# Performance work log

Measured on AMD Instinct MI355X. Metric: run time of the kernel, lower is better.

## Reference

```python
import jax, jax.numpy as jnp
import numpy as np
from jax.ops import segment_sum

N = 100000   # nodes
E = 1600000  # edges
F = 128      # node feature dim
H = 128      # hidden dim
FE = 16      # edge feature dim
G = 256      # num graphs
EPS = 1e-5   # batch-norm eps


def setup_inputs() -> dict:
    key = jax.random.key(0)
    ks = jax.random.split(key, 16)
    s = 0.05
    return {
        "x": jax.random.normal(ks[0], (N, F), jnp.float32),
        "edge_index": jax.random.randint(ks[1], (2, E), 0, N, dtype=jnp.int32),
        "edge_attr": jax.random.normal(ks[2], (E, FE), jnp.float32),
        "batch_idx": jnp.sort(jax.random.randint(ks[3], (N,), 0, G, dtype=jnp.int32)),
        # GCN layer 1
        "W_g1": jax.random.normal(ks[4], (F, H), jnp.float32) * s,
        "b_g1": jnp.zeros((H,), jnp.float32),
        "gamma1": jnp.ones((H,), jnp.float32),
        "beta1": jnp.zeros((H,), jnp.float32),
        # GCN layer 2
        "W_g2": jax.random.normal(ks[5], (H, H), jnp.float32) * s,
        "b_g2": jnp.zeros((H,), jnp.float32),
        "gamma2": jnp.ones((H,), jnp.float32),
        "beta2": jnp.zeros((H,), jnp.float32),
        # edge encoder MLP
        "W_e1": jax.random.normal(ks[6], (FE, H), jnp.float32) * s,
        "b_e1": jnp.zeros((H,), jnp.float32),
        "W_e2": jax.random.normal(ks[7], (H, H), jnp.float32) * s,
        "b_e2": jnp.zeros((H,), jnp.float32),
    }


def _gcn_bn_relu(x, src, dst, W, b, gamma, beta):
    """GCNConv (sym-normalized, self-loops) + BatchNorm1d (batch stats) + ReLU."""
    h = x @ W                                             # [N, H]
    ones = jnp.ones((E,), h.dtype)
    deg = segment_sum(ones, dst, num_segments=N) + 1.0    # self-loop degree
    dinv = jax.lax.rsqrt(deg)                             # [N]
    norm = dinv[src] * dinv[dst]                          # [E]
    agg = segment_sum(h[src] * norm[:, None], dst, num_segments=N)
    out = agg + h * (dinv * dinv)[:, None] + b            # self-loop + bias
    mu = out.mean(axis=0)
    var = out.var(axis=0)
    out = (out - mu) * jax.lax.rsqrt(var + EPS) * gamma + beta
    return jax.nn.relu(out)


def reference(x, edge_index, edge_attr, batch_idx, W_g1, b_g1, gamma1, beta1,
              W_g2, b_g2, gamma2, beta2, W_e1, b_e1, W_e2, b_e2):
    src, dst = edge_index[0], edge_index[1]
    h = _gcn_bn_relu(x, src, dst, W_g1, b_g1, gamma1, beta1)
    h = _gcn_bn_relu(h, src, dst, W_g2, b_g2, gamma2, beta2)

    # global mean pool over nodes per graph
    node_cnt = segment_sum(jnp.ones((N,), h.dtype), batch_idx, num_segments=G)
    graph_repr = segment_sum(h, batch_idx, num_segments=G) / jnp.maximum(node_cnt, 1.0)[:, None]

    # edge encoder MLP + per-graph edge mean (vectorized version of the loop)
    e = jax.nn.relu(edge_attr @ W_e1 + b_e1) @ W_e2 + b_e2   # [E, H]
    edge_batch = batch_idx[src]                              # [E]
    edge_cnt = segment_sum(jnp.ones((E,), e.dtype), edge_batch, num_segments=G)
    edge_sum = segment_sum(e, edge_batch, num_segments=G)
    edge_repr = jnp.where(edge_cnt[:, None] > 0, edge_sum / jnp.maximum(edge_cnt, 1.0)[:, None], 0.0)

    return graph_repr + edge_repr  # [G, H]
```

## Files before the change

### kernel.cpp

```cpp
#include <hip/hip_runtime.h>
#include <cstdint>

__device__ inline unsigned int bfpack2(float a, float b) {
  unsigned int ua = __float_as_uint(a), ub = __float_as_uint(b);
  ua += 0x7FFFu + ((ua >> 16) & 1u);
  ub += 0x7FFFu + ((ub >> 16) & 1u);
  return (ua >> 16) | (ub & 0xFFFF0000u);
}
__device__ inline float bflo(unsigned int u) { return __uint_as_float(u << 16); }
__device__ inline float bfhi(unsigned int u) { return __uint_as_float(u & 0xFFFF0000u); }

__global__ __launch_bounds__(256) void pre_kernel(const int* __restrict__ src,
                                                  const int* __restrict__ dst,
                                                  int* __restrict__ deg,
                                                  int* __restrict__ deg2, int nE) {
  int e = blockIdx.x * 256 + threadIdx.x;
  if (e < nE) {
    atomicAdd(&deg[dst[e]], 1);
    atomicAdd(&deg2[src[e]], 1);
  }
}

__global__ __launch_bounds__(256) void scanA_kernel(const int* __restrict__ deg,
                                                    const int* __restrict__ deg2,
                                                    int* __restrict__ rp,
                                                    int* __restrict__ rp2,
                                                    int* __restrict__ part,
                                                    int* __restrict__ part2,
                                                    int n, int nb) {
  __shared__ int sh[256];
  int b = blockIdx.x, t = threadIdx.x;
  const int* d = (b < nb) ? deg : deg2;
  int* r = (b < nb) ? rp : rp2;
  int* p = (b < nb) ? part : part2;
  int pad = (b < nb) ? 1 : 0;
  int bb = (b < nb) ? b : b - nb;
  int base = bb * 1024 + t * 4;
  int v0 = (base + 0 < n) ? d[base + 0] : 0;
  int v1 = (base + 1 < n) ? d[base + 1] : 0;
  int v2 = (base + 2 < n) ? d[base + 2] : 0;
  int v3 = (base + 3 < n) ? d[base + 3] : 0;
  if (pad) {
    v0 = (v0 + 7) & ~7; v1 = (v1 + 7) & ~7;
    v2 = (v2 + 7) & ~7; v3 = (v3 + 7) & ~7;
  }
  int ts = v0 + v1 + v2 + v3;
  sh[t] = ts;
  __syncthreads();
  for (int off = 1; off < 256; off <<= 1) {
    int x = (t >= off) ? sh[t - off] : 0;
    __syncthreads();
    sh[t] += x;
    __syncthreads();
  }
  int excl = sh[t] - ts;
  if (t == 255) p[bb] = sh[255];
  if (base + 0 < n) r[base + 0] = excl;
  if (base + 1 < n) r[base + 1] = excl + v0;
  if (base + 2 < n) r[base + 2] = excl + v0 + v1;
  if (base + 3 < n) r[base + 3] = excl + v0 + v1 + v2;
}

__global__ void scanB_kernel(int* part, int* part2, int* rp, int* rp2, int nb, int n) {
  if (threadIdx.x == 0) {
    int* p = (blockIdx.x == 0) ? part : part2;
    int* r = (blockIdx.x == 0) ? rp : rp2;
    int run = 0;
    for (int i = 0; i < nb; ++i) { int v = p[i]; p[i] = run; run += v; }
    r[n] = run;
  }
}

__global__ __launch_bounds__(256) void scanC_kernel(int* __restrict__ rp,
                                                    int* __restrict__ rp2,
                                                    const int* __restrict__ part,
                                                    const int* __restrict__ part2,
                                                    int* __restrict__ cursor,
                                                    int* __restrict__ cursor2,
                                                    const int* __restrict__ deg,
                                                    float* __restrict__ dinv, int n) {
  int i = blockIdx.x * 256 + threadIdx.x;
  if (i < n) {
    int v = rp[i] + part[i >> 10];
    rp[i] = v;
    cursor[i] = v;
    dinv[i] = rsqrtf((float)deg[i] + 1.0f);
  } else if (i < 2 * n) {
    int j = i - n;
    int v = rp2[j] + part2[j >> 10];
    rp2[j] = v;
    cursor2[j] = v;
  }
}

template <bool SC>
__global__ __launch_bounds__(256) void placepad_kernel(const int* __restrict__ src,
                                                       const int* __restrict__ dst,
                                                       const int* __restrict__ batch,
                                                       const float* __restrict__ dinv,
                                                       const float* __restrict__ ea,
                                                       int* __restrict__ cursor,
                                                       int* __restrict__ cursor2,
                                                       unsigned int* __restrict__ swp,
                                                       unsigned int* __restrict__ epk,
                                                       int* __restrict__ pos2,
                                                       unsigned int* __restrict__ eah,
                                                       const int* __restrict__ rp,
                                                       const int* __restrict__ deg,
                                                       int nE, int nN) {
  int t = blockIdx.x * 256 + threadIdx.x;
  if (t < nE) {
    int s = src[t];
    int d = dst[t];
    int p1 = atomicAdd(&cursor[d], 1);
    unsigned int fb = __float_as_uint(dinv[s] * dinv[d]);
    fb += 0x7FFFu + ((fb >> 16) & 1u);
    swp[p1] = ((fb >> 16) << 17) | (unsigned int)s;
    int g = batch[s];
    int p2 = atomicAdd(&cursor2[s], 1);
    epk[p2] = ((unsigned int)g << 21) | (unsigned int)t;
    if (SC) {
      const float4* p = reinterpret_cast<const float4*>(ea + (size_t)t * 16);
      float4 a = p[0], b = p[1], c = p[2], dd = p[3];
      uint4 o0, o1;
      o0.x = bfpack2(a.x, a.y); o0.y = bfpack2(a.z, a.w);
      o0.z = bfpack2(b.x, b.y); o0.w = bfpack2(b.z, b.w);
      o1.x = bfpack2(c.x, c.y); o1.y = bfpack2(c.z, c.w);
      o1.z = bfpack2(dd.x, dd.y); o1.w = bfpack2(dd.z, dd.w);
      uint4* dp = reinterpret_cast<uint4*>(eah + (size_t)p2 * 8);
      dp[0] = o0;
      dp[1] = o1;
    } else {
      pos2[t] = p2;
    }
  } else if (t < nE + nN) {
    int i = t - nE;
    int b = rp[i] + deg[i], e = rp[i + 1];
    for (int k = b; k < e; ++k) swp[k] = (unsigned int)i;
  } else if (t < nE + nN + 32) {
    int k = t - nE - nN;
    swp[rp[nN] + k] = 0u;
  }
}

template <bool FUSED>
__global__ __launch_bounds__(256) void gemm128_kernel(const float* __restrict__ A,
                                                      const float* __restrict__ W,
                                                      const float* __restrict__ bs,
                                                      const float* __restrict__ bq,
                                                      const float* __restrict__ gm,
                                                      const float* __restrict__ bt,
                                                      float invN,
                                                      unsigned int* __restrict__ hpk2,
                                                      int nrows) {
  extern __shared__ float lds[];
  float* Ws = lds;
  float* xs = lds + 128 * 128;
  float* scs = xs + 16 * 128;
  float* shs = scs + 128;
  const int t = threadIdx.x;
  for (int i = t; i < (128 * 128) / 4; i += 256)
    reinterpret_cast<float4*>(Ws)[i] = reinterpret_cast<const float4*>(W)[i];
  if (FUSED && t < 128) {
    float mu = bs[t] * invN;
    float var = bq[t] * invN - mu * mu;
    float sc = gm[t] * rsqrtf(var + 1e-5f);
    scs[t] = sc;
    shs[t] = bt[t] - mu * sc;
  }
  const int wave = t >> 6, lane = t & 63;
  const size_t sbase = (size_t)(lane >> 3) * (size_t)nrows * 8 + (lane & 7);
  for (int rb = blockIdx.x * 16; rb < nrows; rb += gridDim.x * 16) {
    int nr = min(16, nrows - rb);
    __syncthreads();
    for (int i = t; i < nr * 32; i += 256) {
      float4 v = reinterpret_cast<const float4*>(A + (size_t)rb * 128)[i];
      if (FUSED) {
        float4 sc4 = reinterpret_cast<const float4*>(scs)[i & 31];
        float4 sh4 = reinterpret_cast<const float4*>(shs)[i & 31];
        v.x = fmaxf(fmaf(v.x, sc4.x, sh4.x), 0.f);
        v.y = fmaxf(fmaf(v.y, sc4.y, sh4.y), 0.f);
        v.z = fmaxf(fmaf(v.z, sc4.z, sh4.z), 0.f);
        v.w = fmaxf(fmaf(v.w, sc4.w, sh4.w), 0.f);
      }
      reinterpret_cast<float4*>(xs)[i] = v;
    }
    __syncthreads();
    float acc[4][2] = {{0.f, 0.f}, {0.f, 0.f}, {0.f, 0.f}, {0.f, 0.f}};
    const float* xw = xs + wave * 4 * 128;
#pragma unroll 4
    for (int k = 0; k < 128; ++k) {
      float w0 = Ws[k * 128 + lane];
      float w1 = Ws[k * 128 + 64 + lane];
#pragma unroll
      for (int r = 0; r < 4; ++r) {
        float a = xw[r * 128 + k];
        acc[r][0] = fmaf(a, w0, acc[r][0]);
        acc[r][1] = fmaf(a, w1, acc[r][1]);
      }
    }
#pragma unroll
    for (int r = 0; r < 4; ++r) {
      int row = rb + wave * 4 + r;
      if (row < nrows)
        hpk2[sbase + (size_t)row * 8] = bfpack2(acc[r][0], acc[r][1]);
    }
  }
}

__global__ __launch_bounds__(256) void spmm8_kernel(const unsigned int* __restrict__ hpk2,
                                                    const float* __restrict__ dinv,
                                                    const int* __restrict__ rp,
                                                    const unsigned int* __restrict__ swp,
                                                    const float* __restrict__ bias,
                                                    float* __restrict__ outp,
                                                    float* __restrict__ bnsum,
                                                    float* __restrict__ bnsq, int nN) {
  const int lane = threadIdx.x & 63;
  const int ch = lane & 7;
  const int es = lane >> 3;
  const int slice = blockIdx.x & 7;
  const unsigned int* hs = hpk2 + (size_t)slice * (size_t)nN * 8;
  const int cb = slice * 8;
  const int wib = (int)(blockIdx.x >> 3) * 4 + (int)(threadIdx.x >> 6);
  const int nws = (int)(gridDim.x >> 3) * 4;
  float b0 = bias[cb + ch], b1 = bias[64 + cb + ch];
  float s0 = 0.f, s1 = 0.f, q0 = 0.f, q1 = 0.f;
  const int half = (nN + 1) >> 1;

#define SPMM_CHUNK(J, ACC0, ACC1)                                         \
  {                                                                       \
    unsigned int v_ = __builtin_nontemporal_load(swp + (J) + es);         \
    unsigned int pp_ = hs[(size_t)(v_ & 0x1FFFFu) * 8 + ch];              \
    float ww_ = __uint_as_float((v_ & 0xFFFE0000u) >> 1);                 \
    ACC0 = fmaf(ww_, bflo(pp_), ACC0);                                    \
    ACC1 = fmaf(ww_, bfhi(pp_), ACC1);                                    \
  }

  for (int p = wib; p < half; p += nws) {
    const int n0 = p;
    const int n1 = p + half;
    const bool has1 = n1 < nN;
    int j0 = rp[n0];
    const int end0 = rp[n0 + 1];
    int j1 = 0, end1 = 0;
    if (has1) { j1 = rp[n1]; end1 = rp[n1 + 1]; }
    float a00 = 0.f, a01 = 0.f, b00 = 0.f, b01 = 0.f;
    float a10 = 0.f, a11 = 0.f, b10 = 0.f, b11 = 0.f;
    while (j0 + 8 < end0 && j1 + 8 < end1) {
      SPMM_CHUNK(j0, a00, a01);
      SPMM_CHUNK(j0 + 8, b00, b01);
      SPMM_CHUNK(j1, a10, a11);
      SPMM_CHUNK(j1 + 8, b10, b11);
      j0 += 16; j1 += 16;
    }
    while (j0 + 8 < end0) {
      SPMM_CHUNK(j0, a00, a01);
      SPMM_CHUNK(j0 + 8, b00, b01);
      j0 += 16;
    }
    if (j0 < end0) SPMM_CHUNK(j0, a00, a01);
    while (j1 + 8 < end1) {
      SPMM_CHUNK(j1, a10, a11);
      SPMM_CHUNK(j1 + 8, b10, b11);
      j1 += 16;
    }
    if (j1 < end1) SPMM_CHUNK(j1, a10, a11);

    a00 += b00; a01 += b01;
    a10 += b10; a11 += b11;
    a00 += __shfl_xor(a00, 8);  a01 += __shfl_xor(a01, 8);
    a10 += __shfl_xor(a10, 8);  a11 += __shfl_xor(a11, 8);
    a00 += __shfl_xor(a00, 16); a01 += __shfl_xor(a01, 16);
    a10 += __shfl_xor(a10, 16); a11 += __shfl_xor(a11, 16);
    a00 += __shfl_xor(a00, 32); a01 += __shfl_xor(a01, 32);
    a10 += __shfl_xor(a10, 32); a11 += __shfl_xor(a11, 32);
    if (es == 0) {
      {
        float dn = dinv[n0];
        float sw = dn * dn;
        unsigned int pn = hs[(size_t)n0 * 8 + ch];
        float o0 = fmaf(bflo(pn), sw, a00) + b0;
        float o1 = fmaf(bfhi(pn), sw, a01) + b1;
        __builtin_nontemporal_store(o0, &outp[(size_t)n0 * 128 + cb + ch]);
        __builtin_nontemporal_store(o1, &outp[(size_t)n0 * 128 + 64 + cb + ch]);
        s0 += o0; s1 += o1;
        q0 = fmaf(o0, o0, q0); q1 = fmaf(o1, o1, q1);
      }
      if (has1) {
        float dn = dinv[n1];
        float sw = dn * dn;
        unsigned int pn = hs[(size_t)n1 * 8 + ch];
        float o0 = fmaf(bflo(pn), sw, a10) + b0;
        float o1 = fmaf(bfhi(pn), sw, a11) + b1;
        __builtin_nontemporal_store(o0, &outp[(size_t)n1 * 128 + cb + ch]);
        __builtin_nontemporal_store(o1, &outp[(size_t)n1 * 128 + 64 + cb + ch]);
        s0 += o0; s1 += o1;
        q0 = fmaf(o0, o0, q0); q1 = fmaf(o1, o1, q1);
      }
    }
  }
#undef SPMM_CHUNK
  if (es == 0) {
    atomicAdd(&bnsum[cb + ch], s0);
    atomicAdd(&bnsum[64 + cb + ch], s1);
    atomicAdd(&bnsq[cb + ch], q0);
    atomicAdd(&bnsq[64 + cb + ch], q1);
  }
}

__global__ __launch_bounds__(256) void pool_kernel(const float* __restrict__ h,
                                                   const int* __restrict__ batch,
                                                   const float* __restrict__ bs,
                                                   const float* __restrict__ bq,
                                                   const float* __restrict__ gm,
                                                   const float* __restrict__ bt,
                                                   float invN,
                                                   float* __restrict__ gsum,
                                                   float* __restrict__ gcnt,
                                                   int nN, int chunk) {
  const int lane = threadIdx.x & 63;
  const int wid = (blockIdx.x * blockDim.x + threadIdx.x) >> 6;
  int beg = wid * chunk;
  if (beg >= nN) return;
  int end = min(nN, beg + chunk);
  const int c2 = 2 * lane;
  float mu0 = bs[c2] * invN, mu1 = bs[c2 + 1] * invN;
  float va0 = bq[c2] * invN - mu0 * mu0, va1 = bq[c2 + 1] * invN - mu1 * mu1;
  float sc0 = gm[c2] * rsqrtf(va0 + 1e-5f), sc1v = gm[c2 + 1] * rsqrtf(va1 + 1e-5f);
  float sh0 = bt[c2] - mu0 * sc0, sh1v = bt[c2 + 1] - mu1 * sc1v;
  int cur = -1;
  float a0 = 0.f, a1 = 0.f, cnt = 0.f;
  for (int n = beg; n < end; ++n) {
    int g = batch[n];
    if (g != cur) {
      if (cur >= 0) {
        atomicAdd(&gsum[cur * 128 + c2], a0);
        atomicAdd(&gsum[cur * 128 + c2 + 1], a1);
        if (lane == 0) atomicAdd(&gcnt[cur], cnt);
      }
      cur = g; a0 = 0.f; a1 = 0.f; cnt = 0.f;
    }
    float2 v = *reinterpret_cast<const float2*>(h + (size_t)n * 128 + c2);
    a0 += fmaxf(fmaf(v.x, sc0, sh0), 0.f);
    a1 += fmaxf(fmaf(v.y, sc1v, sh1v), 0.f);
    cnt += 1.f;
  }
  if (cur >= 0) {
    atomicAdd(&gsum[cur * 128 + c2], a0);
    atomicAdd(&gsum[cur * 128 + c2 + 1], a1);
    if (lane == 0) atomicAdd(&gcnt[cur], cnt);
  }
}

__global__ __launch_bounds__(256) void scatter_kernel(const float* __restrict__ ea,
                                                      const int* __restrict__ pos2,
                                                      unsigned int* __restrict__ eah, int nE) {
  int e = blockIdx.x * 256 + threadIdx.x;
  if (e < nE) {
    const float4* p = reinterpret_cast<const float4*>(ea + (size_t)e * 16);
    float4 a = p[0], b = p[1], c = p[2], d = p[3];
    uint4 o0, o1;
    o0.x = bfpack2(a.x, a.y); o0.y = bfpack2(a.z, a.w);
    o0.z = bfpack2(b.x, b.y); o0.w = bfpack2(b.z, b.w);
    o1.x = bfpack2(c.x, c.y); o1.y = bfpack2(c.z, c.w);
    o1.z = bfpack2(d.x, d.y); o1.w = bfpack2(d.z, d.w);
    int j = pos2[e];
    uint4* dst = reinterpret_cast<uint4*>(eah + (size_t)j * 8);
    dst[0] = o0;
    dst[1] = o1;
  }
}

__global__ __launch_bounds__(256) void edge6_kernel(const unsigned int* __restrict__ eah,
                                                    const unsigned int* __restrict__ epk,
                                                    const float* __restrict__ We1,
                                                    const float* __restrict__ be1,
                                                    float* __restrict__ esum,
                                                    float* __restrict__ ecnt,
                                                    int nE, int chunk) {
  const int lane = threadIdx.x & 63;
  const int wid = (blockIdx.x * 256 + threadIdx.x) >> 6;
  int beg = wid * chunk;
  if (beg >= nE) return;
  int end = min(nE, beg + chunk);
  float w0[16], w1[16];
#pragma unroll
  for (int k = 0; k < 16; ++k) {
    w0[k] = We1[k * 128 + lane];
    w1[k] = We1[k * 128 + 64 + lane];
  }
  float b0 = be1[lane], b1 = be1[64 + lane];
  int cur = -1;
  float a0 = 0.f, a1 = 0.f, cnt = 0.f;
  const uint4* rowp = reinterpret_cast<const uint4*>(eah + (size_t)beg * 8);
  uint4 q0 = rowp[0], q1 = rowp[1];
  int g = (int)(epk[beg] >> 21);
  for (int j = beg; j < end; ++j) {
    uint4 n0, n1;
    int ng = g;
    if (j + 1 < end) {
      const uint4* np = reinterpret_cast<const uint4*>(eah + (size_t)(j + 1) * 8);
      n0 = np[0];
      n1 = np[1];
      ng = (int)(epk[j + 1] >> 21);
    }
    if (g != cur) {
      if (cur >= 0) {
        atomicAdd(&esum[cur * 128 + lane], a0);
        atomicAdd(&esum[cur * 128 + 64 + lane], a1);
        if (lane == 0) atomicAdd(&ecnt[cur], cnt);
      }
      cur = g; a0 = 0.f; a1 = 0.f; cnt = 0.f;
    }
    float u0 = b0, u1 = b1;
    float f;
    f = bflo(q0.x); u0 = fmaf(f, w0[0], u0);  u1 = fmaf(f, w1[0], u1);
    f = bfhi(q0.x); u0 = fmaf(f, w0[1], u0);  u1 = fmaf(f, w1[1], u1);
    f = bflo(q0.y); u0 = fmaf(f, w0[2], u0);  u1 = fmaf(f, w1[2], u1);
    f = bfhi(q0.y); u0 = fmaf(f, w0[3], u0);  u1 = fmaf(f, w1[3], u1);
    f = bflo(q0.z); u0 = fmaf(f, w0[4], u0);  u1 = fmaf(f, w1[4], u1);
    f = bfhi(q0.z); u0 = fmaf(f, w0[5], u0);  u1 = fmaf(f, w1[5], u1);
    f = bflo(q0.w); u0 = fmaf(f, w0[6], u0);  u1 = fmaf(f, w1[6], u1);
    f = bfhi(q0.w); u0 = fmaf(f, w0[7], u0);  u1 = fmaf(f, w1[7], u1);
    f = bflo(q1.x); u0 = fmaf(f, w0[8], u0);  u1 = fmaf(f, w1[8], u1);
    f = bfhi(q1.x); u0 = fmaf(f, w0[9], u0);  u1 = fmaf(f, w1[9], u1);
    f = bflo(q1.y); u0 = fmaf(f, w0[10], u0); u1 = fmaf(f, w1[10], u1);
    f = bfhi(q1.y); u0 = fmaf(f, w0[11], u0); u1 = fmaf(f, w1[11], u1);
    f = bflo(q1.z); u0 = fmaf(f, w0[12], u0); u1 = fmaf(f, w1[12], u1);
    f = bfhi(q1.z); u0 = fmaf(f, w0[13], u0); u1 = fmaf(f, w1[13], u1);
    f = bflo(q1.w); u0 = fmaf(f, w0[14], u0); u1 = fmaf(f, w1[14], u1);
    f = bfhi(q1.w); u0 = fmaf(f, w0[15], u0); u1 = fmaf(f, w1[15], u1);
    a0 += fmaxf(u0, 0.f);
    a1 += fmaxf(u1, 0.f);
    cnt += 1.f;
    q0 = n0; q1 = n1; g = ng;
  }
  if (cur >= 0) {
    atomicAdd(&esum[cur * 128 + lane], a0);
    atomicAdd(&esum[cur * 128 + 64 + lane], a1);
    if (lane == 0) atomicAdd(&ecnt[cur], cnt);
  }
}

__global__ __launch_bounds__(128) void final_kernel(const float* __restrict__ gsum,
                                                    const float* __restrict__ gcnt,
                                                    const float* __restrict__ esum,
                                                    const float* __restrict__ ecnt,
                                                    const float* __restrict__ We2,
                                                    const float* __restrict__ be2,
                                                    float* __restrict__ out) {
  __shared__ float row[128];
  int g = blockIdx.x, c = threadIdx.x;
  row[c] = esum[g * 128 + c];
  __syncthreads();
  float acc = 0.f;
#pragma unroll 4
  for (int k = 0; k < 128; ++k) acc = fmaf(row[k], We2[k * 128 + c], acc);
  float ce = ecnt[g];
  float er = (ce > 0.f) ? (acc / ce + be2[c]) : 0.f;
  float cn = gcnt[g];
  float gr = gsum[g * 128 + c] / fmaxf(cn, 1.f);
  out[g * 128 + c] = gr + er;
}

extern "C" void kernel_launch(void* const* d_in, const int* in_sizes, int n_in,
                              void* d_out, int out_size, void* d_ws, size_t ws_size,
                              hipStream_t stream) {
  const float* x    = (const float*)d_in[0];
  const int*   ei   = (const int*)d_in[1];
  const float* ea   = (const float*)d_in[2];
  const int*   bidx = (const int*)d_in[3];
  const float* Wg1  = (const float*)d_in[4];
  const float* bg1  = (const float*)d_in[5];
  const float* gm1  = (const float*)d_in[6];
  const float* bt1  = (const float*)d_in[7];
  const float* Wg2  = (const float*)d_in[8];
  const float* bg2  = (const float*)d_in[9];
  const float* gm2  = (const float*)d_in[10];
  const float* bt2  = (const float*)d_in[11];
  const float* We1  = (const float*)d_in[12];
  const float* be1  = (const float*)d_in[13];
  const float* We2  = (const float*)d_in[14];
  const float* be2  = (const float*)d_in[15];
  float* out = (float*)d_out;

  const int N = in_sizes[3];
  const int E = in_sizes[1] / 2;
  const int G = out_size / 128;
  const int* srcp = ei;
  const int* dstp = ei + E;
  const int Epad = E + 8 * N;

  char* w = (char*)d_ws;
  auto alloc = [&](size_t b) {
    char* p = w;
    w += (b + 15) & ~(size_t)15;
    return p;
  };
  float* bufB    = (float*)alloc((size_t)N * 128 * 4);
  unsigned int* hpk2 = (unsigned int*)alloc((size_t)N * 64 * 4);
  unsigned int* swp = (unsigned int*)alloc(((size_t)Epad + 32) * 4);
  unsigned int* epk = (unsigned int*)alloc((size_t)E * 4);
  int*   pos2    = (int*)alloc((size_t)E * 4);
  int*   rp      = (int*)alloc((size_t)(N + 1) * 4);
  int*   rp2     = (int*)alloc((size_t)(N + 1) * 4);
  int*   cursor  = (int*)alloc((size_t)N * 4);
  int*   cursor2 = (int*)alloc((size_t)N * 4);
  float* dinv    = (float*)alloc((size_t)N * 4);
  char* zbase = w;
  int*   deg  = (int*)alloc((size_t)N * 4);
  int*   deg2 = (int*)alloc((size_t)N * 4);
  float* bs1  = (float*)alloc(512);
  float* bq1  = (float*)alloc(512);
  float* bs2  = (float*)alloc(512);
  float* bq2  = (float*)alloc(512);
  float* gsum = (float*)alloc((size_t)G * 128 * 4);
  float* gcnt = (float*)alloc((size_t)G * 4);
  float* esum = (float*)alloc((size_t)G * 128 * 4);
  float* ecnt = (float*)alloc((size_t)G * 4);
  int*   part  = (int*)alloc(4096);
  int*   part2 = (int*)alloc(4096);
  size_t zbytes = (size_t)(w - zbase);

  size_t used = (size_t)(w - (char*)d_ws);
  size_t eah_bytes = (size_t)E * 32;
  bool dedicated = (used + eah_bytes + 64) <= ws_size;
  unsigned int* eah = dedicated ? (unsigned int*)alloc(eah_bytes) : (unsigned int*)bufB;

  hipMemsetAsync(zbase, 0, zbytes, stream);

  (void)hipFuncSetAttribute((const void*)gemm128_kernel<false>,
                            hipFuncAttributeMaxDynamicSharedMemorySize, 74752);
  (void)hipFuncSetAttribute((const void*)gemm128_kernel<true>,
                            hipFuncAttributeMaxDynamicSharedMemorySize, 74752);

  pre_kernel<<<(E + 255) / 256, 256, 0, stream>>>(srcp, dstp, deg, deg2, E);
  int nb = (N + 1023) / 1024;
  scanA_kernel<<<2 * nb, 256, 0, stream>>>(deg, deg2, rp, rp2, part, part2, N, nb);
  scanB_kernel<<<2, 64, 0, stream>>>(part, part2, rp, rp2, nb, N);
  scanC_kernel<<<(2 * N + 255) / 256, 256, 0, stream>>>(rp, rp2, part, part2, cursor,
                                                        cursor2, deg, dinv, N);
  int ppg = (E + N + 32 + 255) / 256;
  if (dedicated) {
    placepad_kernel<true><<<ppg, 256, 0, stream>>>(srcp, dstp, bidx, dinv, ea, cursor,
                                                   cursor2, swp, epk, pos2, eah, rp, deg,
                                                   E, N);
  } else {
    placepad_kernel<false><<<ppg, 256, 0, stream>>>(srcp, dstp, bidx, dinv, ea, cursor,
                                                    cursor2, swp, epk, pos2, eah, rp, deg,
                                                    E, N);
  }

  const float invN = 1.0f / (float)N;

  gemm128_kernel<false><<<512, 256, 74752, stream>>>(x, Wg1, nullptr, nullptr, nullptr,
                                                     nullptr, 0.f, hpk2, N);
  spmm8_kernel<<<2048, 256, 0, stream>>>(hpk2, dinv, rp, swp, bg1, bufB, bs1, bq1, N);

  gemm128_kernel<true><<<512, 256, 74752, stream>>>(bufB, Wg2, bs1, bq1, gm1, bt1, invN,
                                                    hpk2, N);
  spmm8_kernel<<<2048, 256, 0, stream>>>(hpk2, dinv, rp, swp, bg2, bufB, bs2, bq2, N);

  int nwp = (2048 * 256) / 64;
  int chunkN = (N + nwp - 1) / nwp;
  pool_kernel<<<2048, 256, 0, stream>>>(bufB, bidx, bs2, bq2, gm2, bt2, invN,
                                        gsum, gcnt, N, chunkN);

  if (!dedicated) {
    scatter_kernel<<<(E + 255) / 256, 256, 0, stream>>>(ea, pos2, eah, E);
  }
  int nwe = (2048 * 256) / 64;
  int chunkE = (E + nwe - 1) / nwe;
  edge6_kernel<<<2048, 256, 0, stream>>>(eah, epk, We1, be1, esum, ecnt, E, chunkE);

  final_kernel<<<G, 128, 0, stream>>>(gsum, gcnt, esum, ecnt, We2, be2, out);
}
```

Before: 1.236 ms.

## Fuse edge encoder work into SpMM launches as extra blocks

Splits the edge-encoder/per-graph edge reduction into two halves and runs each half inside the two SpMM launches, using the first 256 blocks of each launch for edge work and the rest for SpMM. The goal is to overlap the compute-heavy edge MLP with the gather-bound SpMM and remove a separate edge kernel launch. It relies on the dedicated path having filled eah before the SpMMs. The edge blocks compete with SpMM for CUs, and their heavier register use may lower occupancy for the fused kernel.

```diff
diff --git a/kernel.cpp b/kernel.cpp
--- a/kernel.cpp
+++ b/kernel.cpp
@@ -208,22 +208,23 @@
   }
 }
 
-__global__ __launch_bounds__(256) void spmm8_kernel(const unsigned int* __restrict__ hpk2,
-                                                    const float* __restrict__ dinv,
-                                                    const int* __restrict__ rp,
-                                                    const unsigned int* __restrict__ swp,
-                                                    const float* __restrict__ bias,
-                                                    float* __restrict__ outp,
-                                                    float* __restrict__ bnsum,
-                                                    float* __restrict__ bnsq, int nN) {
+__device__ __forceinline__ void spmm_body(const unsigned int* __restrict__ hpk2,
+                                          const float* __restrict__ dinv,
+                                          const int* __restrict__ rp,
+                                          const unsigned int* __restrict__ swp,
+                                          const float* __restrict__ bias,
+                                          float* __restrict__ outp,
+                                          float* __restrict__ bnsum,
+                                          float* __restrict__ bnsq, int nN, int eb) {
   const int lane = threadIdx.x & 63;
   const int ch = lane & 7;
   const int es = lane >> 3;
-  const int slice = blockIdx.x & 7;
+  const int bid = (int)blockIdx.x - eb;
+  const int slice = bid & 7;
   const unsigned int* hs = hpk2 + (size_t)slice * (size_t)nN * 8;
   const int cb = slice * 8;
-  const int wib = (int)(blockIdx.x >> 3) * 4 + (int)(threadIdx.x >> 6);
-  const int nws = (int)(gridDim.x >> 3) * 4;
+  const int wib = (bid >> 3) * 4 + (int)(threadIdx.x >> 6);
+  const int nws = (((int)gridDim.x - eb) >> 3) * 4;
   float b0 = bias[cb + ch], b1 = bias[64 + cb + ch];
   float s0 = 0.f, s1 = 0.f, q0 = 0.f, q1 = 0.f;
   const int half = (nN + 1) >> 1;
@@ -309,6 +310,100 @@
   }
 }
 
+__device__ __forceinline__ void edge_body(const unsigned int* __restrict__ eah,
+                                          const unsigned int* __restrict__ epk,
+                                          const float* __restrict__ We1,
+                                          const float* __restrict__ be1,
+                                          float* __restrict__ esum,
+                                          float* __restrict__ ecnt,
+                                          int eoff, int eend, int chunk) {
+  const int lane = threadIdx.x & 63;
+  const int wid = ((int)blockIdx.x * 256 + (int)threadIdx.x) >> 6;
+  int beg = eoff + wid * chunk;
+  if (beg >= eend) return;
+  int end = min(eend, beg + chunk);
+  float w0[16], w1[16];
+#pragma unroll
+  for (int k = 0; k < 16; ++k) {
+    w0[k] = We1[k * 128 + lane];
+    w1[k] = We1[k * 128 + 64 + lane];
+  }
+  float b0 = be1[lane], b1 = be1[64 + lane];
+  int cur = -1;
+  float a0 = 0.f, a1 = 0.f, cnt = 0.f;
+  const uint4* rowp = reinterpret_cast<const uint4*>(eah + (size_t)beg * 8);
+  uint4 q0 = rowp[0], q1 = rowp[1];
+  int g = (int)(epk[beg] >> 21);
+  for (int j = beg; j < end; ++j) {
+    uint4 n0, n1;
+    int ng = g;
+    if (j + 1 < end) {
+      const uint4* np = reinterpret_cast<const uint4*>(eah + (size_t)(j + 1) * 8);
+      n0 = np[0];
+      n1 = np[1];
+      ng = (int)(epk[j + 1] >> 21);
+    }
+    if (g != cur) {
+      if (cur >= 0) {
+        atomicAdd(&esum[cur * 128 + lane], a0);
+        atomicAdd(&esum[cur * 128 + 64 + lane], a1);
+        if (lane == 0) atomicAdd(&ecnt[cur], cnt);
+      }
+      cur = g; a0 = 0.f; a1 = 0.f; cnt = 0.f;
+    }
+    float u0 = b0, u1 = b1;
+    float f;
+    f = bflo(q0.x); u0 = fmaf(f, w0[0], u0);  u1 = fmaf(f, w1[0], u1);
+    f = bfhi(q0.x); u0 = fmaf(f, w0[1], u0);  u1 = fmaf(f, w1[1], u1);
+    f = bflo(q0.y); u0 = fmaf(f, w0[2], u0);  u1 = fmaf(f, w1[2], u1);
+    f = bfhi(q0.y); u0 = fmaf(f, w0[3], u0);  u1 = fmaf(f, w1[3], u1);
+    f = bflo(q0.z); u0 = fmaf(f, w0[4], u0);  u1 = fmaf(f, w1[4], u1);
+    f = bfhi(q0.z); u0 = fmaf(f, w0[5], u0);  u1 = fmaf(f, w1[5], u1);
+    f = bflo(q0.w); u0 = fmaf(f, w0[6], u0);  u1 = fmaf(f, w1[6], u1);
+    f = bfhi(q0.w); u0 = fmaf(f, w0[7], u0);  u1 = fmaf(f, w1[7], u1);
+    f = bflo(q1.x); u0 = fmaf(f, w0[8], u0);  u1 = fmaf(f, w1[8], u1);
+    f = bfhi(q1.x); u0 = fmaf(f, w0[9], u0);  u1 = fmaf(f, w1[9], u1);
+    f = bflo(q1.y); u0 = fmaf(f, w0[10], u0); u1 = fmaf(f, w1[10], u1);
+    f = bfhi(q1.y); u0 = fmaf(f, w0[11], u0); u1 = fmaf(f, w1[11], u1);
+    f = bflo(q1.z); u0 = fmaf(f, w0[12], u0); u1 = fmaf(f, w1[12], u1);
+    f = bfhi(q1.z); u0 = fmaf(f, w0[13], u0); u1 = fmaf(f, w1[13], u1);
+    f = bflo(q1.w); u0 = fmaf(f, w0[14], u0); u1 = fmaf(f, w1[14], u1);
+    f = bfhi(q1.w); u0 = fmaf(f, w0[15], u0); u1 = fmaf(f, w1[15], u1);
+    a0 += fmaxf(u0, 0.f);
+    a1 += fmaxf(u1, 0.f);
+    cnt += 1.f;
+    q0 = n0; q1 = n1; g = ng;
+  }
+  if (cur >= 0) {
+    atomicAdd(&esum[cur * 128 + lane], a0);
+    atomicAdd(&esum[cur * 128 + 64 + lane], a1);
+    if (lane == 0) atomicAdd(&ecnt[cur], cnt);
+  }
+}
+
+__global__ __launch_bounds__(256) void spmm_edge_kernel(const unsigned int* __restrict__ hpk2,
+                                                        const float* __restrict__ dinv,
+                                                        const int* __restrict__ rp,
+                                                        const unsigned int* __restrict__ swp,
+                                                        const float* __restrict__ bias,
+                                                        float* __restrict__ outp,
+                                                        float* __restrict__ bnsum,
+                                                        float* __restrict__ bnsq, int nN,
+                                                        const unsigned int* __restrict__ eah,
+                                                        const unsigned int* __restrict__ epk,
+                                                        const float* __restrict__ We1,
+                                                        const float* __restrict__ be1,
+                                                        float* __restrict__ esum,
+                                                        float* __restrict__ ecnt,
+                                                        int eoff, int eend, int chunkE,
+                                                        int eb) {
+  if ((int)blockIdx.x < eb) {
+    edge_body(eah, epk, We1, be1, esum, ecnt, eoff, eend, chunkE);
+  } else {
+    spmm_body(hpk2, dinv, rp, swp, bias, outp, bnsum, bnsq, nN, eb);
+  }
+}
+
 __global__ __launch_bounds__(256) void pool_kernel(const float* __restrict__ h,
                                                    const int* __restrict__ batch,
                                                    const float* __restrict__ bs,
@@ -379,68 +474,7 @@
                                                     float* __restrict__ esum,
                                                     float* __restrict__ ecnt,
                                                     int nE, int chunk) {
-  const int lane = threadIdx.x & 63;
-  const int wid = (blockIdx.x * 256 + threadIdx.x) >> 6;
-  int beg = wid * chunk;
-  if (beg >= nE) return;
-  int end = min(nE, beg + chunk);
-  float w0[16], w1[16];
-#pragma unroll
-  for (int k = 0; k < 16; ++k) {
-    w0[k] = We1[k * 128 + lane];
-    w1[k] = We1[k * 128 + 64 + lane];
-  }
-  float b0 = be1[lane], b1 = be1[64 + lane];
-  int cur = -1;
-  float a0 = 0.f, a1 = 0.f, cnt = 0.f;
-  const uint4* rowp = reinterpret_cast<const uint4*>(eah + (size_t)beg * 8);
-  uint4 q0 = rowp[0], q1 = rowp[1];
-  int g = (int)(epk[beg] >> 21);
-  for (int j = beg; j < end; ++j) {
-    uint4 n0, n1;
-    int ng = g;
-    if (j + 1 < end) {
-      const uint4* np = reinterpret_cast<const uint4*>(eah + (size_t)(j + 1) * 8);
-      n0 = np[0];
-      n1 = np[1];
-      ng = (int)(epk[j + 1] >> 21);
-    }
-    if (g != cur) {
-      if (cur >= 0) {
-        atomicAdd(&esum[cur * 128 + lane], a0);
-        atomicAdd(&esum[cur * 128 + 64 + lane], a1);
-        if (lane == 0) atomicAdd(&ecnt[cur], cnt);
-      }
-      cur = g; a0 = 0.f; a1 = 0.f; cnt = 0.f;
-    }
-    float u0 = b0, u1 = b1;
-    float f;
-    f = bflo(q0.x); u0 = fmaf(f, w0[0], u0);  u1 = fmaf(f, w1[0], u1);
-    f = bfhi(q0.x); u0 = fmaf(f, w0[1], u0);  u1 = fmaf(f, w1[1], u1);
-    f = bflo(q0.y); u0 = fmaf(f, w0[2], u0);  u1 = fmaf(f, w1[2], u1);
-    f = bfhi(q0.y); u0 = fmaf(f, w0[3], u0);  u1 = fmaf(f, w1[3], u1);
-    f = bflo(q0.z); u0 = fmaf(f, w0[4], u0);  u1 = fmaf(f, w1[4], u1);
-    f = bfhi(q0.z); u0 = fmaf(f, w0[5], u0);  u1 = fmaf(f, w1[5], u1);
-    f = bflo(q0.w); u0 = fmaf(f, w0[6], u0);  u1 = fmaf(f, w1[6], u1);
-    f = bfhi(q0.w); u0 = fmaf(f, w0[7], u0);  u1 = fmaf(f, w1[7], u1);
-    f = bflo(q1.x); u0 = fmaf(f, w0[8], u0);  u1 = fmaf(f, w1[8], u1);
-    f = bfhi(q1.x); u0 = fmaf(f, w0[9], u0);  u1 = fmaf(f, w1[9], u1);
-    f = bflo(q1.y); u0 = fmaf(f, w0[10], u0); u1 = fmaf(f, w1[10], u1);
-    f = bfhi(q1.y); u0 = fmaf(f, w0[11], u0); u1 = fmaf(f, w1[11], u1);
-    f = bflo(q1.z); u0 = fmaf(f, w0[12], u0); u1 = fmaf(f, w1[12], u1);
-    f = bfhi(q1.z); u0 = fmaf(f, w0[13], u0); u1 = fmaf(f, w1[13], u1);
-    f = bflo(q1.w); u0 = fmaf(f, w0[14], u0); u1 = fmaf(f, w1[14], u1);
-    f = bfhi(q1.w); u0 = fmaf(f, w0[15], u0); u1 = fmaf(f, w1[15], u1);
-    a0 += fmaxf(u0, 0.f);
-    a1 += fmaxf(u1, 0.f);
-    cnt += 1.f;
-    q0 = n0; q1 = n1; g = ng;
-  }
-  if (cur >= 0) {
-    atomicAdd(&esum[cur * 128 + lane], a0);
-    atomicAdd(&esum[cur * 128 + 64 + lane], a1);
-    if (lane == 0) atomicAdd(&ecnt[cur], cnt);
-  }
+  edge_body(eah, epk, We1, be1, esum, ecnt, 0, nE, chunk);
 }
 
 __global__ __launch_bounds__(128) void final_kernel(const float* __restrict__ gsum,
@@ -553,14 +587,22 @@
   }
 
   const float invN = 1.0f / (float)N;
+  const int EB = dedicated ? 256 : 0;
+  const int Ehalf = E / 2;
+  int chunkE1 = EB ? (Ehalf + EB * 4 - 1) / (EB * 4) : 1;
+  int chunkE2 = EB ? ((E - Ehalf) + EB * 4 - 1) / (EB * 4) : 1;
 
   gemm128_kernel<false><<<512, 256, 74752, stream>>>(x, Wg1, nullptr, nullptr, nullptr,
                                                      nullptr, 0.f, hpk2, N);
-  spmm8_kernel<<<2048, 256, 0, stream>>>(hpk2, dinv, rp, swp, bg1, bufB, bs1, bq1, N);
+  spmm_edge_kernel<<<EB + 2048, 256, 0, stream>>>(hpk2, dinv, rp, swp, bg1, bufB, bs1, bq1,
+                                                  N, eah, epk, We1, be1, esum, ecnt,
+                                                  0, EB ? Ehalf : 0, chunkE1, EB);
 
   gemm128_kernel<true><<<512, 256, 74752, stream>>>(bufB, Wg2, bs1, bq1, gm1, bt1, invN,
                                                     hpk2, N);
-  spmm8_kernel<<<2048, 256, 0, stream>>>(hpk2, dinv, rp, swp, bg2, bufB, bs2, bq2, N);
+  spmm_edge_kernel<<<EB + 2048, 256, 0, stream>>>(hpk2, dinv, rp, swp, bg2, bufB, bs2, bq2,
+                                                  N, eah, epk, We1, be1, esum, ecnt,
+                                                  Ehalf, EB ? E : 0, chunkE2, EB);
 
   int nwp = (2048 * 256) / 64;
   int chunkN = (N + nwp - 1) / nwp;
@@ -569,10 +611,10 @@
 
   if (!dedicated) {
     scatter_kernel<<<(E + 255) / 256, 256, 0, stream>>>(ea, pos2, eah, E);
-  }
-  int nwe = (2048 * 256) / 64;
-  int chunkE = (E + nwe - 1) / nwe;
-  edge6_kernel<<<2048, 256, 0, stream>>>(eah, epk, We1, be1, esum, ecnt, E, chunkE);
+    int nwe = (2048 * 256) / 64;
+    int chunkE = (E + nwe - 1) / nwe;
+    edge6_kernel<<<2048, 256, 0, stream>>>(eah, epk, We1, be1, esum, ecnt, E, chunkE);
+  }
 
   final_kernel<<<G, 128, 0, stream>>>(gsum, gcnt, esum, ecnt, We2, be2, out);
 }
```

New measurement: 1.368 ms. 10.6% more time.
